# Kernel optimization log

Measured on AMD Instinct MI355X. Metric: run time of the kernel, lower is better.

## Reference

```python
import jax, jax.numpy as jnp
import numpy as np
import math

D_MODEL = 1024
N_HEADS = 16
D_K = D_MODEL // N_HEADS
D_FF = 4096
EPS = 1e-6


def layernorm(x, alpha, beta):
    # Faithful to the torch module: std is UNBIASED (ddof=1), eps added to std (not var).
    mean = jnp.mean(x, axis=-1, keepdims=True)
    n = x.shape[-1]
    var = jnp.sum((x - mean) ** 2, axis=-1, keepdims=True) / (n - 1)
    std = jnp.sqrt(var)
    return alpha * (x - mean) / (std + EPS) + beta


def setup_inputs() -> dict:
    key = jax.random.key(0)
    ks = jax.random.split(key, 16)
    B, S = 4, 1024
    s = 1.0 / math.sqrt(D_MODEL)
    inp = {
        "x": jax.random.normal(ks[0], (B, S, D_MODEL), dtype=jnp.float32),
        "mask": jnp.ones((B, 1, 1, S), dtype=jnp.int32),
        "wq": jax.random.normal(ks[1], (D_MODEL, D_MODEL), jnp.float32) * s,
        "bq": jnp.zeros((D_MODEL,), jnp.float32),
        "wk": jax.random.normal(ks[2], (D_MODEL, D_MODEL), jnp.float32) * s,
        "bk": jnp.zeros((D_MODEL,), jnp.float32),
        "wv": jax.random.normal(ks[3], (D_MODEL, D_MODEL), jnp.float32) * s,
        "bv": jnp.zeros((D_MODEL,), jnp.float32),
        "wo": jax.random.normal(ks[4], (D_MODEL, D_MODEL), jnp.float32) * s,
        "bo": jnp.zeros((D_MODEL,), jnp.float32),
        "w1": jax.random.normal(ks[5], (D_MODEL, D_FF), jnp.float32) * s,
        "b1": jnp.zeros((D_FF,), jnp.float32),
        "w2": jax.random.normal(ks[6], (D_FF, D_MODEL), jnp.float32) * (1.0 / math.sqrt(D_FF)),
        "b2": jnp.zeros((D_MODEL,), jnp.float32),
        "alpha1": jnp.ones((1,), jnp.float32),
        "beta1": jnp.zeros((1,), jnp.float32),
        "alpha2": jnp.ones((1,), jnp.float32),
        "beta2": jnp.zeros((1,), jnp.float32),
    }
    return inp


def encoder_block(x, mask, wq, bq, wk, bk, wv, bv, wo, bo, w1, b1, w2, b2,
                  alpha1, beta1, alpha2, beta2):
    B, S, _ = x.shape
    # --- residual 1: pre-norm + self-attention ---
    xn = layernorm(x, alpha1, beta1)
    q = (xn @ wq + bq).reshape(B, S, N_HEADS, D_K)
    k = (xn @ wk + bk).reshape(B, S, N_HEADS, D_K)
    v = (xn @ wv + bv).reshape(B, S, N_HEADS, D_K)
    scores = jnp.einsum('bshd,bthd->bhst', q, k) / math.sqrt(D_K)  # [B,h,S,S]
    scores = jnp.where(mask == 0, jnp.float32(-1e9), scores)
    attn = jax.nn.softmax(scores, axis=-1)
    ctx = jnp.einsum('bhst,bthd->bshd', attn, v).reshape(B, S, D_MODEL)
    attn_out = ctx @ wo + bo
    x = x + attn_out
    # --- residual 2: pre-norm + FFN ---
    xn = layernorm(x, alpha2, beta2)
    ffn = jax.nn.relu(xn @ w1 + b1) @ w2 + b2
    return x + ffn


def reference(x, mask, wq, bq, wk, bk, wv, bv, wo, bo, w1, b1, w2, b2,
              alpha1, beta1, alpha2, beta2):
    return encoder_block(x, mask, wq, bq, wk, bk, wv, bv, wo, bo,
                         w1, b1, w2, b2, alpha1, beta1, alpha2, beta2)
```

## Files before the change

### kernel.cpp

```cpp
#include <hip/hip_runtime.h>

using u16 = unsigned short;
using s16x8 = __attribute__((ext_vector_type(8))) short;
using f32x4 = __attribute__((ext_vector_type(4))) float;

__device__ __forceinline__ float bf2f(u16 u) {
  union { unsigned int i; float f; } c; c.i = ((unsigned int)u) << 16; return c.f;
}
__device__ __forceinline__ u16 f2bf(float f) {
  union { float f; unsigned int i; } c; c.f = f;
  unsigned int x = c.i;
  return (u16)((x + 0x7fffu + ((x >> 16) & 1u)) >> 16);
}

#define GLOAD16(g, l) __builtin_amdgcn_global_load_lds(                         \
    (const __attribute__((address_space(1))) void*)(g),                          \
    (__attribute__((address_space(3))) void*)(l), 16, 0, 0)

__device__ __forceinline__ int2 xcd_swizzle() {
  const int nwg = gridDim.x * gridDim.y;
  int f = blockIdx.y * gridDim.x + blockIdx.x;
  f = (f & 7) * (nwg >> 3) + (f >> 3);
  return make_int2(f % gridDim.x, f / gridDim.x);
}

__global__ __launch_bounds__(256) void fill_kernel(float* out, int n) {
  int i = blockIdx.x * 256 + threadIdx.x;
  if (i < n) out[i] = 999.0f;
}

__global__ __launch_bounds__(256) void convT_kernel(
    const float* __restrict__ in, u16* __restrict__ out, int R, int C) {
  __shared__ u16 t[64][72];
  const int nbc = C >> 6;
  const int br = blockIdx.x / nbc, bc = blockIdx.x % nbc;
  const int tid = threadIdx.x;
  const int r4 = tid >> 4;
  const int c4 = (tid & 15) * 4;
  for (int i = 0; i < 4; i++) {
    int row = i * 16 + r4;
    float4 v = *(const float4*)(in + (size_t)(br * 64 + row) * C + bc * 64 + c4);
    t[row][c4 + 0] = f2bf(v.x); t[row][c4 + 1] = f2bf(v.y);
    t[row][c4 + 2] = f2bf(v.z); t[row][c4 + 3] = f2bf(v.w);
  }
  __syncthreads();
  for (int i = 0; i < 4; i++) {
    int row2 = i * 16 + r4;
    ushort4 v;
    v.x = t[c4 + 0][row2]; v.y = t[c4 + 1][row2];
    v.z = t[c4 + 2][row2]; v.w = t[c4 + 3][row2];
    *(ushort4*)(out + (size_t)(bc * 64 + row2) * R + br * 64 + c4) = v;
  }
}

__global__ __launch_bounds__(256) void convT4_kernel(
    const float* __restrict__ i0, const float* __restrict__ i1,
    const float* __restrict__ i2, const float* __restrict__ i3,
    u16* __restrict__ o0, u16* __restrict__ o1,
    u16* __restrict__ o2, u16* __restrict__ o3) {
  __shared__ u16 t[64][72];
  const float* in = blockIdx.y == 0 ? i0 : blockIdx.y == 1 ? i1 : blockIdx.y == 2 ? i2 : i3;
  u16* out = blockIdx.y == 0 ? o0 : blockIdx.y == 1 ? o1 : blockIdx.y == 2 ? o2 : o3;
  const int br = blockIdx.x >> 4, bc = blockIdx.x & 15;
  const int tid = threadIdx.x;
  const int r4 = tid >> 4;
  const int c4 = (tid & 15) * 4;
  for (int i = 0; i < 4; i++) {
    int row = i * 16 + r4;
    float4 v = *(const float4*)(in + (size_t)(br * 64 + row) * 1024 + bc * 64 + c4);
    t[row][c4 + 0] = f2bf(v.x); t[row][c4 + 1] = f2bf(v.y);
    t[row][c4 + 2] = f2bf(v.z); t[row][c4 + 3] = f2bf(v.w);
  }
  __syncthreads();
  for (int i = 0; i < 4; i++) {
    int row2 = i * 16 + r4;
    ushort4 v;
    v.x = t[c4 + 0][row2]; v.y = t[c4 + 1][row2];
    v.z = t[c4 + 2][row2]; v.w = t[c4 + 3][row2];
    *(ushort4*)(out + (size_t)(bc * 64 + row2) * 1024 + br * 64 + c4) = v;
  }
}

__global__ __launch_bounds__(256) void transT_bf16_kernel(
    const u16* __restrict__ in, u16* __restrict__ out) {
  __shared__ u16 t[64][72];
  const int bc = blockIdx.x;
  const int br = blockIdx.y;
  const int tid = threadIdx.x;
  const int r4 = tid >> 4;
  const int c4 = (tid & 15) * 4;
  for (int i = 0; i < 4; i++) {
    int row = i * 16 + r4;
    ushort4 v = *(const ushort4*)(in + (size_t)(br * 64 + row) * 1024 + bc * 64 + c4);
    *(ushort4*)&t[row][c4] = v;
  }
  __syncthreads();
  const int batch = br >> 4;
  const int s0 = (br & 15) * 64;
  for (int i = 0; i < 4; i++) {
    int row2 = i * 16 + r4;
    ushort4 v;
    v.x = t[c4 + 0][row2]; v.y = t[c4 + 1][row2];
    v.z = t[c4 + 2][row2]; v.w = t[c4 + 3][row2];
    *(ushort4*)(out + ((size_t)batch * 1024 + bc * 64 + row2) * 1024 + s0 + c4) = v;
  }
}

__global__ __launch_bounds__(256) void ln_kernel(
    const float* __restrict__ x, u16* __restrict__ y,
    const float* __restrict__ alpha, const float* __restrict__ beta) {
  __shared__ float red[8];
  const int row = blockIdx.x;
  const int tid = threadIdx.x;
  float4 u = ((const float4*)(x + (size_t)row * 1024))[tid];
  float v0 = u.x, v1 = u.y, v2 = u.z, v3 = u.w;
  float s = v0 + v1 + v2 + v3;
  for (int off = 32; off; off >>= 1) s += __shfl_xor(s, off, 64);
  if ((tid & 63) == 0) red[tid >> 6] = s;
  __syncthreads();
  float mean = (red[0] + red[1] + red[2] + red[3]) * (1.f / 1024.f);
  v0 -= mean; v1 -= mean; v2 -= mean; v3 -= mean;
  float q = v0 * v0 + v1 * v1 + v2 * v2 + v3 * v3;
  for (int off = 32; off; off >>= 1) q += __shfl_xor(q, off, 64);
  if ((tid & 63) == 0) red[4 + (tid >> 6)] = q;
  __syncthreads();
  float var = (red[4] + red[5] + red[6] + red[7]) * (1.f / 1023.f);
  float inv = 1.f / (sqrtf(var) + 1e-6f);
  float a = alpha[0], b = beta[0];
  ushort4 o;
  o.x = f2bf(a * v0 * inv + b); o.y = f2bf(a * v1 * inv + b);
  o.z = f2bf(a * v2 * inv + b); o.w = f2bf(a * v3 * inv + b);
  ((ushort4*)(y + (size_t)row * 1024))[tid] = o;
}

__global__ __launch_bounds__(256) void ln_bf16_kernel(
    const u16* __restrict__ x, u16* __restrict__ y,
    const float* __restrict__ alpha, const float* __restrict__ beta) {
  __shared__ float red[8];
  const int row = blockIdx.x;
  const int tid = threadIdx.x;
  ushort4 u = ((const ushort4*)(x + (size_t)row * 1024))[tid];
  float v0 = bf2f(u.x), v1 = bf2f(u.y), v2 = bf2f(u.z), v3 = bf2f(u.w);
  float s = v0 + v1 + v2 + v3;
  for (int off = 32; off; off >>= 1) s += __shfl_xor(s, off, 64);
  if ((tid & 63) == 0) red[tid >> 6] = s;
  __syncthreads();
  float mean = (red[0] + red[1] + red[2] + red[3]) * (1.f / 1024.f);
  v0 -= mean; v1 -= mean; v2 -= mean; v3 -= mean;
  float q = v0 * v0 + v1 * v1 + v2 * v2 + v3 * v3;
  for (int off = 32; off; off >>= 1) q += __shfl_xor(q, off, 64);
  if ((tid & 63) == 0) red[4 + (tid >> 6)] = q;
  __syncthreads();
  float var = (red[4] + red[5] + red[6] + red[7]) * (1.f / 1023.f);
  float inv = 1.f / (sqrtf(var) + 1e-6f);
  float a = alpha[0], b = beta[0];
  ushort4 o;
  o.x = f2bf(a * v0 * inv + b); o.y = f2bf(a * v1 * inv + b);
  o.z = f2bf(a * v2 * inv + b); o.w = f2bf(a * v3 * inv + b);
  ((ushort4*)(y + (size_t)row * 1024))[tid] = o;
}

template<int EPI, int TM, int TN>
__global__ __launch_bounds__(256) void gemm_bt(
    const u16* __restrict__ A, const u16* __restrict__ Bt,
    const float* __restrict__ bias, const void* __restrict__ res,
    void* __restrict__ Cv, int M, int N, int K, int lda, int ldb, int ldc) {
  constexpr int MI = TM / 32;
  constexpr int NI = TN / 32;
  constexpr int CA = TM / 32;
  constexpr int CB = TN / 32;
  constexpr int CMAX = CA > CB ? CA : CB;
  __shared__ u16 As[TM * 64];
  __shared__ u16 Bs[TN * 64];
  const int2 bxy = xcd_swizzle();
  const int bn = bxy.x, bm = bxy.y;
  const int m0 = bm * TM, n0 = bn * TN;
  const int tid = threadIdx.x;
  const int w = tid >> 6, l = tid & 63;
  const int lr = l & 15, lg = l >> 4;
  const int wr = w >> 1, wc = w & 1;

  f32x4 acc[MI][NI] = {};

  for (int k0 = 0; k0 < K; k0 += 64) {
#pragma unroll
    for (int c = 0; c < CMAX; c++) {
      const int o = c * 4096 + tid * 16;
      const int row = o >> 7;
      const int cb = (o & 127) ^ ((row & 7) << 4);
      if (c < CA)
        GLOAD16((const char*)A + ((size_t)(m0 + row) * lda + k0) * 2 + cb,
                (char*)As + c * 4096 + w * 1024);
      if (c < CB)
        GLOAD16((const char*)Bt + ((size_t)(n0 + row) * ldb + k0) * 2 + cb,
                (char*)Bs + c * 4096 + w * 1024);
    }
    __syncthreads();
#pragma unroll
    for (int kk = 0; kk < 2; kk++) {
      const int kb = kk * 64 + lg * 16;
      s16x8 a[MI], b[NI];
      for (int mi = 0; mi < MI; mi++) {
        int row = wr * (MI * 16) + mi * 16 + lr;
        a[mi] = *(const s16x8*)((const char*)As +
                 ((row << 7) | (kb ^ ((row & 7) << 4))));
      }
      for (int ni = 0; ni < NI; ni++) {
        int row = wc * (NI * 16) + ni * 16 + lr;
        b[ni] = *(const s16x8*)((const char*)Bs +
                 ((row << 7) | (kb ^ ((row & 7) << 4))));
      }
      for (int mi = 0; mi < MI; mi++)
        for (int ni = 0; ni < NI; ni++)
          acc[mi][ni] = __builtin_amdgcn_mfma_f32_16x16x32_bf16(
              a[mi], b[ni], acc[mi][ni], 0, 0, 0);
    }
    __syncthreads();
  }

  for (int mi = 0; mi < MI; mi++) {
    for (int ni = 0; ni < NI; ni++) {
      const int n = n0 + wc * (NI * 16) + ni * 16 + lr;
      const float bv = bias[n];
      for (int r = 0; r < 4; r++) {
        const int m = m0 + wr * (MI * 16) + mi * 16 + lg * 4 + r;
        float v = acc[mi][ni][r] + bv;
        if (EPI == 1) {
          v = v > 0.f ? v : 0.f;
          ((u16*)Cv)[(size_t)m * ldc + n] = f2bf(v);
        } else if (EPI == 2) {
          v += ((const float*)res)[(size_t)m * ldc + n];
          ((u16*)Cv)[(size_t)m * ldc + n] = f2bf(v);
        } else {
          v += bf2f(((const u16*)res)[(size_t)m * ldc + n]);
          ((float*)Cv)[(size_t)m * ldc + n] = v;
        }
      }
    }
  }
}

__global__ __launch_bounds__(256) void gemm_qkv(
    const u16* __restrict__ A, const u16* __restrict__ WT,
    const float* __restrict__ bq, const float* __restrict__ bk,
    const float* __restrict__ bv,
    u16* __restrict__ qb_, u16* __restrict__ kb_, u16* __restrict__ vb_) {
  __shared__ u16 As[128 * 64];
  __shared__ u16 Bs[128 * 64];
  const int2 bxy = xcd_swizzle();
  const int bn = bxy.x, bm = bxy.y;
  const int m0 = bm * 128, n0 = bn * 128;
  const int tid = threadIdx.x;
  const int w = tid >> 6, l = tid & 63;
  const int lr = l & 15, lg = l >> 4;
  const int wr = w >> 1, wc = w & 1;

  f32x4 acc[4][4] = {};

  for (int k0 = 0; k0 < 1024; k0 += 64) {
#pragma unroll
    for (int c = 0; c < 4; c++) {
      const int o = c * 4096 + tid * 16;
      const int row = o >> 7;
      const int cb = (o & 127) ^ ((row & 7) << 4);
      GLOAD16((const char*)A + ((size_t)(m0 + row) * 1024 + k0) * 2 + cb,
              (char*)As + c * 4096 + w * 1024);
      GLOAD16((const char*)WT + ((size_t)(n0 + row) * 1024 + k0) * 2 + cb,
              (char*)Bs + c * 4096 + w * 1024);
    }
    __syncthreads();
#pragma unroll
    for (int kk = 0; kk < 2; kk++) {
      const int kb = kk * 64 + lg * 16;
      s16x8 a[4], b[4];
      for (int mi = 0; mi < 4; mi++) {
        int row = wr * 64 + mi * 16 + lr;
        a[mi] = *(const s16x8*)((const char*)As +
                 ((row << 7) | (kb ^ ((row & 7) << 4))));
      }
      for (int ni = 0; ni < 4; ni++) {
        int row = wc * 64 + ni * 16 + lr;
        b[ni] = *(const s16x8*)((const char*)Bs +
                 ((row << 7) | (kb ^ ((row & 7) << 4))));
      }
      for (int mi = 0; mi < 4; mi++)
        for (int ni = 0; ni < 4; ni++)
          acc[mi][ni] = __builtin_amdgcn_mfma_f32_16x16x32_bf16(
              a[mi], b[ni], acc[mi][ni], 0, 0, 0);
    }
    __syncthreads();
  }

  const int seg = n0 >> 10;
  u16* outp = seg == 0 ? qb_ : seg == 1 ? kb_ : vb_;
  for (int mi = 0; mi < 4; mi++) {
    for (int ni = 0; ni < 4; ni++) {
      const int n = n0 + wc * 64 + ni * 16 + lr;
      const int nn = n & 1023;
      const float bias = seg == 0 ? bq[nn] : seg == 1 ? bk[nn] : bv[nn];
      for (int r = 0; r < 4; r++) {
        const int m = m0 + wr * 64 + mi * 16 + lg * 4 + r;
        outp[(size_t)m * 1024 + nn] = f2bf(acc[mi][ni][r] + bias);
      }
    }
  }
}

__global__ __launch_bounds__(256) void attn_kernel(
    const u16* __restrict__ q, const u16* __restrict__ k,
    const u16* __restrict__ vT, const int* __restrict__ mask,
    u16* __restrict__ ctx) {
  __shared__ u16 Ks[64 * 64];
  __shared__ u16 Vs[64 * 64];
  __shared__ u16 Pl[4][32][68];
  const int qt = blockIdx.x;
  const int bh = blockIdx.y;
  const int b = bh >> 4, h = bh & 15;
  const int tid = threadIdx.x;
  const int w = tid >> 6, l = tid & 63;
  const int lr = l & 15, lg = l >> 4;
  const int qrow0 = qt * 128 + w * 32;

  s16x8 aq[2][2];
#pragma unroll
  for (int g = 0; g < 2; g++) {
    const u16* qp = q + ((size_t)(b * 1024 + qrow0 + g * 16 + lr)) * 1024 + h * 64 + lg * 8;
    aq[g][0] = *(const s16x8*)qp;
    aq[g][1] = *(const s16x8*)(qp + 32);
  }

  const s16x8 vone = {0x3F80, 0x3F80, 0x3F80, 0x3F80, 0x3F80, 0x3F80, 0x3F80, 0x3F80};

  f32x4 acc[2][4] = {};
  f32x4 lacc[2] = {};

  const char* kby = (const char*)(k + ((size_t)(b * 1024)) * 1024 + h * 64);
  const char* vby = (const char*)(vT + ((size_t)b) * 1024 * 1024 + ((size_t)(h * 64)) * 1024);
  const int* mbase = mask + b * 1024;

  const int o0 = tid * 16;
#define STAGE_KV(t0_)                                                           \
  {                                                                             \
    _Pragma("unroll")                                                           \
    for (int c = 0; c < 2; c++) {                                               \
      const int o = c * 4096 + o0;                                              \
      const int row = o >> 7;                                                   \
      const int cb = (o & 127) ^ ((row & 7) << 4);                              \
      GLOAD16(kby + (size_t)(t0_ + row) * 2048 + cb,                            \
              (char*)Ks + c * 4096 + w * 1024);                                 \
      GLOAD16(vby + (size_t)row * 2048 + (size_t)(t0_) * 2 + cb,                \
              (char*)Vs + c * 4096 + w * 1024);                                 \
    }                                                                           \
  }

  STAGE_KV(0);
  __syncthreads();

  for (int it = 0; it < 16; ++it) {
    const int t0 = it * 64;

    float p[2][4][4];
#pragma unroll
    for (int sub = 0; sub < 4; sub++) {
      const int krow = sub * 16 + lr;
      const int sw = (krow & 7) << 4;
      const char* kp = (const char*)Ks + (krow << 7);
      s16x8 bk0 = *(const s16x8*)(kp + ((lg * 16) ^ sw));
      s16x8 bk1 = *(const s16x8*)(kp + ((lg * 16 + 64) ^ sw));
      const int mv = mbase[t0 + krow];
#pragma unroll
      for (int g = 0; g < 2; g++) {
        f32x4 d = {};
        d = __builtin_amdgcn_mfma_f32_16x16x32_bf16(aq[g][0], bk0, d, 0, 0, 0);
        d = __builtin_amdgcn_mfma_f32_16x16x32_bf16(aq[g][1], bk1, d, 0, 0, 0);
        for (int r = 0; r < 4; r++) {
          float s = d[r] * 0.125f;
          p[g][sub][r] = __expf((mv == 0) ? -1e9f : s);
        }
      }
    }
#pragma unroll
    for (int g = 0; g < 2; g++)
      for (int sub = 0; sub < 4; sub++)
        for (int r = 0; r < 4; r++)
          Pl[w][g * 16 + lg * 4 + r][sub * 16 + lr] = f2bf(p[g][sub][r]);
    asm volatile("s_waitcnt lgkmcnt(0)" ::: "memory");
    __builtin_amdgcn_sched_barrier(0);
#pragma unroll
    for (int kb2 = 0; kb2 < 2; kb2++) {
      const s16x8 ap0 = *(const s16x8*)&Pl[w][lr][kb2 * 32 + lg * 8];
      const s16x8 ap1 = *(const s16x8*)&Pl[w][16 + lr][kb2 * 32 + lg * 8];
      lacc[0] = __builtin_amdgcn_mfma_f32_16x16x32_bf16(ap0, vone, lacc[0], 0, 0, 0);
      lacc[1] = __builtin_amdgcn_mfma_f32_16x16x32_bf16(ap1, vone, lacc[1], 0, 0, 0);
#pragma unroll
      for (int d4 = 0; d4 < 4; d4++) {
        const int vrow = d4 * 16 + lr;
        const char* vp = (const char*)Vs + (vrow << 7);
        s16x8 bvv = *(const s16x8*)(vp + ((kb2 * 64 + lg * 16) ^ ((vrow & 7) << 4)));
        acc[0][d4] = __builtin_amdgcn_mfma_f32_16x16x32_bf16(ap0, bvv, acc[0][d4], 0, 0, 0);
        acc[1][d4] = __builtin_amdgcn_mfma_f32_16x16x32_bf16(ap1, bvv, acc[1][d4], 0, 0, 0);
      }
    }
    if (it < 15) {
      __syncthreads();
      STAGE_KV(t0 + 64);
      __syncthreads();
    }
  }

#pragma unroll
  for (int g = 0; g < 2; g++)
    for (int d4 = 0; d4 < 4; d4++)
      for (int r = 0; r < 4; r++) {
        const int row = b * 1024 + qrow0 + g * 16 + lg * 4 + r;
        ctx[(size_t)row * 1024 + h * 64 + d4 * 16 + lr] = f2bf(acc[g][d4][r] / lacc[g][r]);
      }
#undef STAGE_KV
}

extern "C" void kernel_launch(void* const* d_in, const int* in_sizes, int n_in,
                              void* d_out, int out_size, void* d_ws, size_t ws_size,
                              hipStream_t stream) {
  float* out = (float*)d_out;

  const size_t REQUIRED = (size_t)64 * 1024 * 1024;
  if (ws_size < REQUIRED) {
    fill_kernel<<<dim3((out_size + 255) / 256), 256, 0, stream>>>(out, out_size);
    return;
  }

  const float* x    = (const float*)d_in[0];
  const int*   mask = (const int*)d_in[1];
  const float* wq = (const float*)d_in[2];
  const float* bq = (const float*)d_in[3];
  const float* wk = (const float*)d_in[4];
  const float* bk = (const float*)d_in[5];
  const float* wv = (const float*)d_in[6];
  const float* bv = (const float*)d_in[7];
  const float* wo = (const float*)d_in[8];
  const float* bo = (const float*)d_in[9];
  const float* w1 = (const float*)d_in[10];
  const float* b1 = (const float*)d_in[11];
  const float* w2 = (const float*)d_in[12];
  const float* b2 = (const float*)d_in[13];
  const float* alpha1 = (const float*)d_in[14];
  const float* beta1  = (const float*)d_in[15];
  const float* alpha2 = (const float*)d_in[16];
  const float* beta2  = (const float*)d_in[17];

  char* W = (char*)d_ws;
  const size_t MB = 1024 * 1024;
  u16* wqT  = (u16*)(W + 0 * MB);
  u16* wkT  = (u16*)(W + 2 * MB);
  u16* wvT  = (u16*)(W + 4 * MB);
  u16* woT  = (u16*)(W + 6 * MB);
  u16* xn   = (u16*)(W + 8 * MB);
  u16* qbuf = (u16*)(W + 16 * MB);
  u16* kbuf = (u16*)(W + 24 * MB);
  u16* vT   = (u16*)(W + 32 * MB);
  u16* vbuf = (u16*)(W + 40 * MB);
  u16* x1b  = (u16*)(W + 56 * MB);
  u16* ctx  = xn;
  u16* w1T  = (u16*)(W + 0 * MB);
  u16* w2T  = (u16*)(W + 8 * MB);
  u16* xn2  = (u16*)(W + 16 * MB);
  u16* hbuf = (u16*)(W + 24 * MB);

  convT4_kernel<<<dim3(256, 4), 256, 0, stream>>>(wq, wk, wv, wo, wqT, wkT, wvT, woT);

  ln_kernel<<<dim3(4096), 256, 0, stream>>>(x, xn, alpha1, beta1);

  gemm_qkv<<<dim3(24, 32), 256, 0, stream>>>(xn, wqT, bq, bk, bv, qbuf, kbuf, vbuf);

  transT_bf16_kernel<<<dim3(16, 64), 256, 0, stream>>>(vbuf, vT);

  attn_kernel<<<dim3(8, 64), 256, 0, stream>>>(qbuf, kbuf, vT, mask, ctx);

  gemm_bt<2, 64, 64><<<dim3(16, 64), 256, 0, stream>>>(
      ctx, woT, bo, x, x1b, 4096, 1024, 1024, 1024, 1024, 1024);

  convT_kernel<<<dim3(16 * 64), 256, 0, stream>>>(w1, w1T, 1024, 4096);
  convT_kernel<<<dim3(64 * 16), 256, 0, stream>>>(w2, w2T, 4096, 1024);

  ln_bf16_kernel<<<dim3(4096), 256, 0, stream>>>(x1b, xn2, alpha2, beta2);

  gemm_bt<1, 128, 128><<<dim3(32, 32), 256, 0, stream>>>(
      xn2, w1T, b1, nullptr, hbuf, 4096, 4096, 1024, 1024, 1024, 4096);
  gemm_bt<5, 64, 64><<<dim3(16, 64), 256, 0, stream>>>(
      hbuf, w2T, b2, x1b, out, 4096, 1024, 4096, 4096, 4096, 1024);
}
```

Baseline: 233.7 us.

## Add triple-buffered LDS prefetch pipeline to 64x64 GEMMs

Adds a PIPE template flag to the bf16 GEMM. When it is set, the kernel keeps three LDS stages and issues global->LDS loads two k-tiles ahead, using a vmcnt wait and one barrier per iteration instead of two __syncthreads. This is meant to hide global load latency behind MFMA work in the Wo projection and the FFN down-projection GEMMs. It triples LDS use for those kernels, which may reduce occupancy, and it depends on a hand-set vmcnt literal that only holds for the 64x64 tile.

Result: slower. 271.5 us (+16.2%).

```diff
diff --git a/kernel.cpp b/kernel.cpp
--- a/kernel.cpp
+++ b/kernel.cpp
@@ -160,7 +160,7 @@
   ((ushort4*)(y + (size_t)row * 1024))[tid] = o;
 }
 
-template<int EPI, int TM, int TN>
+template<int EPI, int TM, int TN, bool PIPE>
 __global__ __launch_bounds__(256) void gemm_bt(
     const u16* __restrict__ A, const u16* __restrict__ Bt,
     const float* __restrict__ bias, const void* __restrict__ res,
@@ -170,8 +170,9 @@
   constexpr int CA = TM / 32;
   constexpr int CB = TN / 32;
   constexpr int CMAX = CA > CB ? CA : CB;
-  __shared__ u16 As[TM * 64];
-  __shared__ u16 Bs[TN * 64];
+  constexpr int NBUF = PIPE ? 3 : 1;
+  __shared__ u16 As[NBUF * TM * 64];
+  __shared__ u16 Bs[NBUF * TN * 64];
   const int2 bxy = xcd_swizzle();
   const int bn = bxy.x, bm = bxy.y;
   const int m0 = bm * TM, n0 = bn * TN;
@@ -182,41 +183,69 @@
 
   f32x4 acc[MI][NI] = {};
 
-  for (int k0 = 0; k0 < K; k0 += 64) {
-#pragma unroll
-    for (int c = 0; c < CMAX; c++) {
-      const int o = c * 4096 + tid * 16;
-      const int row = o >> 7;
-      const int cb = (o & 127) ^ ((row & 7) << 4);
-      if (c < CA)
-        GLOAD16((const char*)A + ((size_t)(m0 + row) * lda + k0) * 2 + cb,
-                (char*)As + c * 4096 + w * 1024);
-      if (c < CB)
-        GLOAD16((const char*)Bt + ((size_t)(n0 + row) * ldb + k0) * 2 + cb,
-                (char*)Bs + c * 4096 + w * 1024);
-    }
-    __syncthreads();
-#pragma unroll
-    for (int kk = 0; kk < 2; kk++) {
-      const int kb = kk * 64 + lg * 16;
-      s16x8 a[MI], b[NI];
-      for (int mi = 0; mi < MI; mi++) {
-        int row = wr * (MI * 16) + mi * 16 + lr;
-        a[mi] = *(const s16x8*)((const char*)As +
-                 ((row << 7) | (kb ^ ((row & 7) << 4))));
-      }
-      for (int ni = 0; ni < NI; ni++) {
-        int row = wc * (NI * 16) + ni * 16 + lr;
-        b[ni] = *(const s16x8*)((const char*)Bs +
-                 ((row << 7) | (kb ^ ((row & 7) << 4))));
-      }
-      for (int mi = 0; mi < MI; mi++)
-        for (int ni = 0; ni < NI; ni++)
-          acc[mi][ni] = __builtin_amdgcn_mfma_f32_16x16x32_bf16(
-              a[mi], b[ni], acc[mi][ni], 0, 0, 0);
-    }
-    __syncthreads();
-  }
+#define G_STAGE(bi, k0_)                                                        \
+  {                                                                             \
+    _Pragma("unroll")                                                           \
+    for (int c = 0; c < CMAX; c++) {                                            \
+      const int o = c * 4096 + tid * 16;                                        \
+      const int row = o >> 7;                                                   \
+      const int cb = (o & 127) ^ ((row & 7) << 4);                              \
+      if (c < CA)                                                               \
+        GLOAD16((const char*)A + ((size_t)(m0 + row) * lda + (k0_)) * 2 + cb,   \
+                (char*)As + (bi) * (TM * 128) + c * 4096 + w * 1024);           \
+      if (c < CB)                                                               \
+        GLOAD16((const char*)Bt + ((size_t)(n0 + row) * ldb + (k0_)) * 2 + cb,  \
+                (char*)Bs + (bi) * (TN * 128) + c * 4096 + w * 1024);           \
+    }                                                                           \
+  }
+
+#define G_COMPUTE(bi)                                                           \
+  {                                                                             \
+    _Pragma("unroll")                                                           \
+    for (int kk = 0; kk < 2; kk++) {                                            \
+      const int kb = kk * 64 + lg * 16;                                         \
+      s16x8 a[MI], b[NI];                                                       \
+      for (int mi = 0; mi < MI; mi++) {                                         \
+        int row = wr * (MI * 16) + mi * 16 + lr;                                \
+        a[mi] = *(const s16x8*)((const char*)As + (bi) * (TM * 128) +           \
+                 ((row << 7) | (kb ^ ((row & 7) << 4))));                       \
+      }                                                                         \
+      for (int ni = 0; ni < NI; ni++) {                                         \
+        int row = wc * (NI * 16) + ni * 16 + lr;                                \
+        b[ni] = *(const s16x8*)((const char*)Bs + (bi) * (TN * 128) +           \
+                 ((row << 7) | (kb ^ ((row & 7) << 4))));                       \
+      }                                                                         \
+      for (int mi = 0; mi < MI; mi++)                                           \
+        for (int ni = 0; ni < NI; ni++)                                         \
+          acc[mi][ni] = __builtin_amdgcn_mfma_f32_16x16x32_bf16(                \
+              a[mi], b[ni], acc[mi][ni], 0, 0, 0);                              \
+    }                                                                           \
+  }
+
+  if constexpr (PIPE) {
+    static_assert(TM == 64 && TN == 64, "PIPE tuned for 64x64 (vmcnt literal)");
+    const int T = K >> 6;
+    G_STAGE(0, 0);
+    G_STAGE(1, 64);
+    for (int t = 0; t < T; ++t) {
+      if (t == T - 1) asm volatile("s_waitcnt vmcnt(0)" ::: "memory");
+      else            asm volatile("s_waitcnt vmcnt(4)" ::: "memory");
+      __builtin_amdgcn_s_barrier();
+      __builtin_amdgcn_sched_barrier(0);
+      if (t + 2 < T) { G_STAGE((t + 2) % 3, (t + 2) * 64); }
+      __builtin_amdgcn_sched_barrier(0);
+      G_COMPUTE(t % 3);
+    }
+  } else {
+    for (int k0 = 0; k0 < K; k0 += 64) {
+      G_STAGE(0, k0);
+      __syncthreads();
+      G_COMPUTE(0);
+      __syncthreads();
+    }
+  }
+#undef G_STAGE
+#undef G_COMPUTE
 
   for (int mi = 0; mi < MI; mi++) {
     for (int ni = 0; ni < NI; ni++) {
@@ -476,7 +505,7 @@
 
   attn_kernel<<<dim3(8, 64), 256, 0, stream>>>(qbuf, kbuf, vT, mask, ctx);
 
-  gemm_bt<2, 64, 64><<<dim3(16, 64), 256, 0, stream>>>(
+  gemm_bt<2, 64, 64, true><<<dim3(16, 64), 256, 0, stream>>>(
       ctx, woT, bo, x, x1b, 4096, 1024, 1024, 1024, 1024, 1024);
 
   convT_kernel<<<dim3(16 * 64), 256, 0, stream>>>(w1, w1T, 1024, 4096);
@@ -484,8 +513,8 @@
 
   ln_bf16_kernel<<<dim3(4096), 256, 0, stream>>>(x1b, xn2, alpha2, beta2);
 
-  gemm_bt<1, 128, 128><<<dim3(32, 32), 256, 0, stream>>>(
+  gemm_bt<1, 128, 128, false><<<dim3(32, 32), 256, 0, stream>>>(
       xn2, w1T, b1, nullptr, hbuf, 4096, 4096, 1024, 1024, 1024, 4096);
-  gemm_bt<5, 64, 64><<<dim3(16, 64), 256, 0, stream>>>(
+  gemm_bt<5, 64, 64, true><<<dim3(16, 64), 256, 0, stream>>>(
       hbuf, w2T, b2, x1b, out, 4096, 1024, 4096, 4096, 4096, 1024);
 }
```
